# Optimization experiments

Measured on AMD Instinct MI355X. Metric: run time of the kernel, lower is better.

## Reference

```python
import jax, jax.numpy as jnp
import numpy as np


def setup_inputs() -> dict:
    key = jax.random.key(0)
    k1, k2, k3, k4, k5, k6 = jax.random.split(key, 6)
    B, V = 128, 128000
    logits = jax.random.normal(k1, (B, V), dtype=jnp.float32) * 2.0
    # keep temperatures away from 0 to avoid overflow in logits/temp
    temperatures = 0.7 + 0.6 * jax.random.uniform(k2, (B,), dtype=jnp.float32)
    top_ks = jax.random.randint(k3, (B,), 1, 1024, dtype=jnp.int32)
    top_ps = 0.7 + 0.29 * jax.random.uniform(k4, (B,), dtype=jnp.float32)
    min_ps = 0.02 * jax.random.uniform(k5, (B,), dtype=jnp.float32)
    # uniform variate for inverse-CDF multinomial sampling (one sample per row)
    u = jax.random.uniform(k6, (B, 1), dtype=jnp.float32)
    return {
        "logits": logits,
        "temperatures": temperatures,
        "top_ks": top_ks,
        "top_ps": top_ps,
        "min_ps": min_ps,
        "u": u,
    }


def reference(logits, temperatures, top_ks, top_ps, min_ps, u):
    """Faithful jax version of Sampler's torch-native sampling path:
    softmax(logits/T) -> descending sort -> top-k mask -> top-p mask
    (cumsum computed pre-mask, exactly as torch code) -> min-p mask ->
    multinomial sample (inverse CDF with provided uniform u) ->
    gather original token index. Also returns the renormalized filtered
    probs scattered back to vocab order (top_p_normalize_probs-style)."""
    B, V = logits.shape
    probs = jax.nn.softmax(logits / temperatures[:, None], axis=-1)  # [B, V]

    order = jnp.argsort(-probs, axis=-1)                     # descending indices
    probs_sort = jnp.take_along_axis(probs, order, axis=-1)  # [B, V] sorted desc
    probs_sum = jnp.cumsum(probs_sort, axis=-1)              # cumsum BEFORE masking

    pos = jnp.arange(V, dtype=jnp.int32)[None, :]
    # top-k: zero everything at rank >= top_k
    probs_sort = jnp.where(pos >= top_ks[:, None], 0.0, probs_sort)
    # top-p: zero where cumulative mass strictly before this token exceeds top_p
    probs_sort = jnp.where(probs_sum - probs_sort > top_ps[:, None], 0.0, probs_sort)
    # min-p: threshold relative to the max prob (rank-0 entry survives both masks)
    min_p_thr = probs_sort[:, :1] * min_ps[:, None]
    probs_sort = jnp.where(probs_sort < min_p_thr, 0.0, probs_sort)

    total = jnp.sum(probs_sort, axis=-1, keepdims=True)      # [B, 1]
    cdf = jnp.cumsum(probs_sort, axis=-1) / total            # normalized CDF
    # inverse-CDF sampling == torch.multinomial(probs_sort, 1)
    sampled_rank = jnp.clip(jnp.sum(cdf < u, axis=-1, keepdims=True), 0, V - 1)
    token_ids = jnp.take_along_axis(order, sampled_rank, axis=-1)[:, 0].astype(jnp.int32)

    # scatter renormalized filtered probs back to original vocab positions
    inv_order = jnp.argsort(order, axis=-1)
    norm_probs = jnp.take_along_axis(probs_sort / total, inv_order, axis=-1)
    return token_ids, norm_probs
```

## Files before the change

### kernel.cpp

```cpp
#include <hip/hip_runtime.h>
#include <stdint.h>
#include <math.h>

#define T0 256
#define T1 512
#define TPB 1024
#define NB 2048
#define SPLIT 8
#define NW 8
#define LW 256
#define NSEG (SPLIT*NW)
#define CAND2 2048
#define PS0 2048
#define L2E 1.44269504088896f

typedef float vfloat4 __attribute__((ext_vector_type(4)));
typedef unsigned long long ull;

__device__ __forceinline__ unsigned fkey(float f) {
    unsigned u = __float_as_uint(f);
    return (u & 0x80000000u) ? ~u : (u | 0x80000000u);
}
__device__ __forceinline__ float funkey(unsigned k) {
    unsigned u = (k & 0x80000000u) ? (k ^ 0x80000000u) : ~k;
    return __uint_as_float(u);
}
__device__ __forceinline__ ull packkv(unsigned k, unsigned idx) {
    return ((ull)k << 32) | (ull)(~idx);
}

__device__ __forceinline__ void suffix_scan_2048(unsigned* h, unsigned* wscr, int tid)
{
    const int lane = tid & 63, w = tid >> 6;
    const int i0 = 2047 - 2 * tid;
    const int i1 = 2046 - 2 * tid;
    unsigned a = h[i0], b = h[i1];
    unsigned s = a + b;
    unsigned inc = s;
    #pragma unroll
    for (int d = 1; d < 64; d <<= 1) { unsigned o = __shfl_up(inc, d); if (lane >= d) inc += o; }
    if (lane == 63) wscr[w] = inc;
    __syncthreads();
    if (w == 0) {
        unsigned v = (lane < 16) ? wscr[lane] : 0u;
        unsigned vi = v;
        #pragma unroll
        for (int d = 1; d < 16; d <<= 1) { unsigned o = __shfl_up(vi, d); if (lane >= d) vi += o; }
        if (lane < 16) wscr[16 + lane] = vi - v;
    }
    __syncthreads();
    unsigned off = wscr[16 + w] + (inc - s);
    h[i0] = off + a;
    h[i1] = off + a + b;
    __syncthreads();
}

__global__ __launch_bounds__(T0)
void k0_cut(const float* __restrict__ logits,
            const float* __restrict__ temps,
            const int* __restrict__ top_ks,
            float* __restrict__ ws_cy,
            unsigned* __restrict__ ws_cut,
            int V, int Vq)
{
    const int slot = blockIdx.x;
    const int b = slot / SPLIT, s = slot % SPLIT;
    const int tid = threadIdx.x, lane = tid & 63, w = tid >> 6;
    const int start = s * Vq;
    const int len = min(Vq, V - start);

    __shared__ unsigned hist[NB];
    __shared__ unsigned uscr[16];
    __shared__ float fred[8];
    __shared__ int bstar;

    if (len <= 0) {
        if (tid == 0) { ws_cut[slot] = 0xFFFFFFFFu; ws_cy[slot] = -1e30f; }
        return;
    }
    for (int i = tid; i < NB; i += T0) hist[i] = 0;
    if (tid == 0) bstar = 0;
    __syncthreads();

    const float* __restrict__ row = logits + (size_t)b * V + start;
    const vfloat4* __restrict__ row4 = (const vfloat4*)row;
    const int nps = min(len, PS0);
    const int np4 = nps >> 2;

    float m0 = -1e30f;
    for (int i = tid; i < np4; i += T0) {
        vfloat4 v = row4[i];
        #pragma unroll
        for (int j = 0; j < 4; ++j) {
            float lv = v[j];
            m0 = fmaxf(m0, lv);
            atomicAdd(&hist[fkey(lv) >> 21], 1u);
        }
    }
    for (int i = (np4 << 2) + tid; i < nps; i += T0) {
        float lv = row[i];
        m0 = fmaxf(m0, lv);
        atomicAdd(&hist[fkey(lv) >> 21], 1u);
    }
    #pragma unroll
    for (int d = 32; d > 0; d >>= 1) m0 = fmaxf(m0, __shfl_down(m0, d));
    if (lane == 0) fred[w] = m0;
    __syncthreads();
    if (tid == 0) {
        float mm = fred[0];
        for (int j = 1; j < T0 / 64; ++j) mm = fmaxf(mm, fred[j]);
        fred[4] = mm;
    }
    __syncthreads();
    const float m0max = fred[4];

    unsigned sloc[8];
    unsigned acc = 0;
    #pragma unroll
    for (int j = 0; j < 8; ++j) { acc += hist[2047 - (8 * tid + j)]; sloc[j] = acc; }
    __syncthreads();
    unsigned inc = acc;
    #pragma unroll
    for (int d = 1; d < 64; d <<= 1) { unsigned o = __shfl_up(inc, d); if (lane >= d) inc += o; }
    if (lane == 63) uscr[w] = inc;
    __syncthreads();
    if (tid == 0) {
        unsigned o = 0;
        for (int j = 0; j < T0 / 64; ++j) { unsigned t = uscr[j]; uscr[8 + j] = o; o += t; }
    }
    __syncthreads();
    unsigned off = uscr[8 + w] + (inc - acc);
    #pragma unroll
    for (int j = 0; j < 8; ++j) hist[2047 - (8 * tid + j)] = off + sloc[j];
    __syncthreads();

    int K = top_ks[b]; K = max(K, 1); K = min(K, 1024);
    float sexp = (float)K * (float)nps / (float)V;
    unsigned TGT = (unsigned)(sexp + 6.0f * sqrtf(sexp) + 16.5f);
    if (TGT > (unsigned)nps) TGT = (unsigned)nps;
    for (int e = tid; e < NB; e += T0) {
        unsigned Se = hist[e];
        unsigned Sn = (e < NB - 1) ? hist[e + 1] : 0u;
        if (Se >= TGT && Sn < TGT) bstar = e;
    }
    __syncthreads();
    if (tid == 0) {
        ws_cut[slot] = (unsigned)bstar << 21;
        ws_cy[slot]  = m0max / temps[b];
    }
}

__global__ __launch_bounds__(T1)
void k1_scan(const float* __restrict__ logits,
             const float* __restrict__ temps,
             float* __restrict__ out_probs,
             const float* __restrict__ ws_cy,
             const unsigned* __restrict__ ws_cut,
             float* __restrict__ ws_z,
             unsigned* __restrict__ ws_wcnt,
             unsigned* __restrict__ ws_maxk,
             ull* __restrict__ ws_cand,
             int V, int Vq)
{
    const int slot = blockIdx.x;
    const int b = slot / SPLIT, s = slot % SPLIT;
    const int tid = threadIdx.x, lane = tid & 63, wv = tid >> 6;
    const int start = s * Vq;
    const int len = min(Vq, V - start);

    __shared__ float fred[2 * NW];
    __shared__ unsigned ucnt[NW];

    if (len <= 0) {
        if (lane == 0) ws_wcnt[slot * NW + wv] = 0u;
        if (tid == 0) { ws_z[slot] = 0.0f; ws_maxk[slot] = 0u; }
        return;
    }

    const float invT = 1.0f / temps[b];
    const float Cy = ws_cy[slot];
    const float cutval = funkey(ws_cut[slot]);

    const float* __restrict__ row = logits + (size_t)b * V + start;
    const vfloat4* __restrict__ row4 = (const vfloat4*)row;
    const int L4 = len >> 2;

    {
        float* __restrict__ orow = out_probs + (size_t)b * V + start;
        vfloat4* __restrict__ orow4 = (vfloat4*)orow;
        const vfloat4 z4 = (vfloat4)0.0f;
        for (int i = tid; i < L4; i += T1) orow4[i] = z4;
        for (int i = (L4 << 2) + tid; i < len; i += T1) orow[i] = 0.0f;
    }

    const float ca = invT * L2E;
    const float cb = -Cy * L2E;
    ull* gw = ws_cand + ((size_t)slot * NW + wv) * LW;
    const ull lmask = (1ull << lane) - 1ull;

    unsigned wcnt = 0;
    float z0 = 0.0f, z1 = 0.0f, z2 = 0.0f, z3 = 0.0f, mb = -1e30f;

    #define E4(v) (exp2f(fmaf((v)[0], ca, cb)) + exp2f(fmaf((v)[1], ca, cb)) \
                 + exp2f(fmaf((v)[2], ca, cb)) + exp2f(fmaf((v)[3], ca, cb)))
    #define GE1(x, gi) do {                                                 \
        bool p = (x) >= cutval;                                             \
        ull bm = __ballot(p);                                               \
        if (bm) {                                                           \
            mb = fmaxf(mb, p ? (x) : -1e30f);                               \
            unsigned pos = wcnt + (unsigned)__popcll(bm & lmask);           \
            if (p && pos < LW) gw[pos] = packkv(fkey(x), (unsigned)(gi));   \
            wcnt += (unsigned)__popcll(bm);                                 \
        }                                                                   \
    } while (0)
    #define GE4(v, ii) do {                                                 \
        unsigned gbase = (unsigned)(start + ((ii) << 2));                   \
        GE1((v)[0], gbase + 0); GE1((v)[1], gbase + 1);                     \
        GE1((v)[2], gbase + 2); GE1((v)[3], gbase + 3);                     \
    } while (0)

    int k = 0;
    for (; (k + 4) * T1 <= L4; k += 4) {
        int i0 = k * T1 + tid;
        vfloat4 va = row4[i0];
        vfloat4 vb = row4[i0 + T1];
        vfloat4 vc = row4[i0 + 2 * T1];
        vfloat4 vd = row4[i0 + 3 * T1];
        z0 += E4(va); z1 += E4(vb); z2 += E4(vc); z3 += E4(vd);
        GE4(va, i0); GE4(vb, i0 + T1); GE4(vc, i0 + 2 * T1); GE4(vd, i0 + 3 * T1);
    }
    for (; k * T1 + (wv << 6) < L4; ++k) {
        int idx = k * T1 + tid;
        vfloat4 v = (idx < L4) ? row4[idx] : (vfloat4)(-1e30f);
        z0 += E4(v);
        GE4(v, idx);
    }
    for (int j = (L4 << 2) + tid; j < len; j += T1) {
        float lv = row[j];
        z0 += exp2f(fmaf(lv, ca, cb));
        GE1(lv, start + j);
    }
    #undef E4
    #undef GE1
    #undef GE4

    float z = (z0 + z1) + (z2 + z3);
    #pragma unroll
    for (int d = 32; d > 0; d >>= 1) {
        z += __shfl_down(z, d);
        mb = fmaxf(mb, __shfl_down(mb, d));
    }
    if (lane == 0) {
        fred[wv] = z; fred[NW + wv] = mb; ucnt[wv] = wcnt;
        ws_wcnt[slot * NW + wv] = wcnt;
    }
    __syncthreads();
    if (tid == 0) {
        float zz = 0.0f, mm = -1e30f; unsigned tot = 0;
        for (int j = 0; j < NW; ++j) { zz += fred[j]; mm = fmaxf(mm, fred[NW + j]); tot += ucnt[j]; }
        ws_z[slot] = zz;
        ws_maxk[slot] = tot ? fkey(mm) : 0u;
    }
}

__global__ __launch_bounds__(TPB)
void k2_sample(const float* __restrict__ logits,
               const float* __restrict__ temps,
               const int* __restrict__ top_ks,
               const float* __restrict__ top_ps,
               const float* __restrict__ min_ps,
               const float* __restrict__ uvec,
               const float* __restrict__ ws_cy,
               const float* __restrict__ ws_z,
               const unsigned* __restrict__ ws_cut,
               const unsigned* __restrict__ ws_wcnt,
               const unsigned* __restrict__ ws_maxk,
               const ull* __restrict__ ws_cand,
               float* __restrict__ out_tok,
               float* __restrict__ out_probs,
               int V)
{
    const int b = blockIdx.x;
    const int tid = threadIdx.x, lane = tid & 63, w = tid >> 6;
    const float invT = 1.0f / temps[b];
    int Korig = top_ks[b]; Korig = max(Korig, 1); Korig = min(Korig, 1024);
    const unsigned Ku = (unsigned)Korig;
    const float top_p = top_ps[b], min_p = min_ps[b], uval = uvec[b];

    __shared__ __align__(16) char smem[53760];
    ull*            cand  = (ull*)(smem);
    ull*            cand2 = (ull*)(smem + 16384);
    unsigned*       hist  = (unsigned*)(smem + 32768);
    unsigned short* cnts  = (unsigned short*)(smem + 41216);
    float*          sh_p  = (float*)(smem + 45312);
    float*          sh_c  = (float*)(smem + 49408);
    unsigned short* segc  = (unsigned short*)(smem + 53504);
    __shared__ unsigned uscr[32];
    __shared__ float fws[32];
    __shared__ unsigned scnt;
    __shared__ int sh_i1, sh_i2;
    __shared__ unsigned sh_u1;

    bool myfb = false;
    for (int i = tid; i < NSEG; i += TPB) {
        unsigned c = ws_wcnt[b * NSEG + i];
        if (c > (unsigned)LW) myfb = true;
        segc[i] = (unsigned short)min(c, (unsigned)LW);
    }
    float Cy[SPLIT], zq[SPLIT];
    unsigned cutq[SPLIT], mkq[SPLIT];
    #pragma unroll
    for (int q = 0; q < SPLIT; ++q) {
        int sl = b * SPLIT + q;
        Cy[q] = ws_cy[sl]; zq[q] = ws_z[sl];
        cutq[q] = ws_cut[sl]; mkq[q] = ws_maxk[sl];
    }
    __syncthreads();
    unsigned cntq[SPLIT];
    #pragma unroll
    for (int q = 0; q < SPLIT; ++q) {
        unsigned t = 0;
        #pragma unroll
        for (int v = 0; v < NW; ++v) t += segc[q * NW + v];
        cntq[q] = t;
    }
    float Y = -1e30f;
    #pragma unroll
    for (int q = 0; q < SPLIT; ++q) if (zq[q] > 0.0f) Y = fmaxf(Y, Cy[q]);
    float Z = 0.0f;
    #pragma unroll
    for (int q = 0; q < SPLIT; ++q)
        if (zq[q] > 0.0f) Z += zq[q] * exp2f((Cy[q] - Y) * L2E);

    unsigned cutmax = 0, mincut = 0xFFFFFFFFu, maxkey = 0;
    #pragma unroll
    for (int q = 0; q < SPLIT; ++q) {
        if (cntq[q] > 0u) {
            if (!isfinite(zq[q])) myfb = true;
            cutmax = max(cutmax, cutq[q]);
            mincut = min(mincut, cutq[q]);
            maxkey = max(maxkey, mkq[q]);
        }
    }
    if (mincut == 0xFFFFFFFFu || !isfinite(Z) || Z <= 0.0f) myfb = true;
    bool fb = __syncthreads_or((int)myfb) != 0;

    unsigned Tkeyb = 0;
    int count = 0, bstar = 0, shift = 0;
    const unsigned base = mincut;
    const ull* cbase = ws_cand + (size_t)b * NSEG * LW;

    if (!fb) {
        const unsigned range = maxkey - base;
        while ((range >> shift) > (unsigned)(NB - 1)) shift++;
        for (int i = tid; i <= NB; i += TPB) hist[i] = 0;
        if (tid == 0) { sh_i1 = -1; scnt = 0; }
        __syncthreads();
        for (int v = tid; v < NSEG * LW; v += TPB) {
            int off = v & (LW - 1);
            int seg = v >> 8;
            if (off < (int)segc[seg]) {
                ull e = cbase[v];
                atomicAdd(&hist[((unsigned)(e >> 32) - base) >> shift], 1u);
            }
        }
        __syncthreads();
        unsigned fat = 0;
        for (int i = tid; i < NB; i += TPB) {
            unsigned h = hist[i];
            cnts[i] = (unsigned short)h;
            fat = max(fat, h);
        }
        #pragma unroll
        for (int d = 32; d > 0; d >>= 1) fat = max(fat, __shfl_down(fat, d));
        if (lane == 0) uscr[w] = fat;
        __syncthreads();
        if (tid == 0) {
            unsigned m2 = 0;
            for (int j = 0; j < 16; ++j) m2 = max(m2, uscr[j]);
            uscr[16] = m2;
        }
        __syncthreads();
        if (uscr[16] > 64u) fb = true;
    }
    if (!fb) {
        suffix_scan_2048(hist, uscr, tid);
        for (int e = tid; e < NB; e += TPB) {
            unsigned Se = hist[e], Sn = (e < NB - 1) ? hist[e + 1] : 0u;
            if (Se >= Ku && Sn < Ku) { sh_i1 = e; sh_u1 = Se; }
        }
        __syncthreads();
        if (sh_i1 < 0) fb = true;
        else {
            bstar = sh_i1;
            count = (int)sh_u1;
            Tkeyb = base + ((unsigned)bstar << shift);
            if (Tkeyb < cutmax || count > CAND2) fb = true;
        }
    }
    if (!fb) {
        for (int v = tid; v < NSEG * LW; v += TPB) {
            int off = v & (LW - 1);
            int seg = v >> 8;
            if (off < (int)segc[seg]) {
                ull e = cbase[v];
                unsigned k = (unsigned)(e >> 32);
                if (k >= Tkeyb) {
                    unsigned bin = (k - base) >> shift;
                    unsigned pos = atomicAdd(&hist[bin + 1], 1u);
                    cand2[pos] = e;
                }
            }
        }
        __syncthreads();
        for (int e = bstar + tid; e < NB; e += TPB) {
            int c = (int)cnts[e];
            if (c >= 2) {
                int st = (int)hist[e + 1] - c;
                for (int x = 1; x < c; ++x) {
                    ull key = cand2[st + x];
                    int y = x - 1;
                    while (y >= 0 && cand2[st + y] < key) { cand2[st + y + 1] = cand2[st + y]; --y; }
                    cand2[st + y + 1] = key;
                }
            }
        }
        __syncthreads();
    }

    if (fb) {
        const float* __restrict__ row = logits + (size_t)b * V;
        float m = -1e30f, z = 0.0f;
        for (int i = tid; i < V; i += TPB) {
            float y = row[i] * invT;
            float nm = fmaxf(m, y);
            z = z * exp2f((m - nm) * L2E) + exp2f((y - nm) * L2E);
            m = nm;
        }
        sh_p[tid] = m; sh_c[tid] = z;
        __syncthreads();
        for (int d = TPB >> 1; d > 0; d >>= 1) {
            if (tid < d) {
                float m1 = sh_p[tid], z1 = sh_c[tid];
                float m2 = sh_p[tid + d], z2 = sh_c[tid + d];
                float mm = fmaxf(m1, m2);
                sh_c[tid] = z1 * exp2f((m1 - mm) * L2E) + z2 * exp2f((m2 - mm) * L2E);
                sh_p[tid] = mm;
            }
            __syncthreads();
        }
        Y = sh_p[0]; Z = sh_c[0];
        __syncthreads();
        for (int i = tid; i < NB; i += TPB) hist[i] = 0;
        if (tid == 0) { sh_i1 = 0; sh_i2 = 0; sh_u1 = 0; }
        __syncthreads();
        for (int i = tid; i < V; i += TPB) atomicAdd(&hist[fkey(row[i]) >> 21], 1u);
        __syncthreads();
        suffix_scan_2048(hist, uscr, tid);
        for (int e = tid; e < NB; e += TPB) {
            unsigned Se = hist[e], Sn = (e < NB-1) ? hist[e+1] : 0u;
            if (Se >= Ku && Sn < Ku) { sh_i1 = e; sh_u1 = Sn; }
        }
        __syncthreads();
        int b1 = sh_i1;
        unsigned cab = sh_u1;
        for (int i = tid; i < NB; i += TPB) hist[i] = 0;
        __syncthreads();
        for (int i = tid; i < V; i += TPB) {
            unsigned k = fkey(row[i]);
            if ((int)(k >> 21) == b1) atomicAdd(&hist[(k >> 10) & (NB - 1)], 1u);
        }
        __syncthreads();
        suffix_scan_2048(hist, uscr, tid);
        for (int e = tid; e < NB; e += TPB) {
            unsigned Se = cab + hist[e];
            unsigned Sn = cab + ((e < NB-1) ? hist[e+1] : 0u);
            if (Se >= Ku && Sn < Ku) sh_i2 = e;
        }
        __syncthreads();
        unsigned Tkey = ((unsigned)b1 << 21) | ((unsigned)sh_i2 << 10);
        if (tid == 0) scnt = 0;
        __syncthreads();
        for (int i = tid; i < V; i += TPB) {
            unsigned k = fkey(row[i]);
            if (k >= Tkey) {
                unsigned pos = atomicAdd(&scnt, 1u);
                if (pos < CAND2) cand[pos] = packkv(k, (unsigned)i);
            }
        }
        __syncthreads();
        count = (scnt < (unsigned)CAND2) ? (int)scnt : CAND2;

        int n_sort = 1;
        while (n_sort < count) n_sort <<= 1;
        for (int i = tid; i < n_sort; i += TPB)
            if (i >= count) cand[i] = 0ull;
        __syncthreads();
        for (int kk = 2; kk <= n_sort; kk <<= 1) {
            for (int j = kk >> 1; j > 0; j >>= 1) {
                for (int i = tid; i < n_sort; i += TPB) {
                    int ixj = i ^ j;
                    if (ixj > i) {
                        ull a = cand[i], c = cand[ixj];
                        bool up = (i & kk) == 0;
                        if (up ? (a < c) : (a > c)) { cand[i] = c; cand[ixj] = a; }
                    }
                }
                __syncthreads();
            }
        }
    }

    ull* srt = fb ? cand : cand2;
    int K = min(Korig, count);

    float pv = 0.0f;
    if (tid < K) {
        unsigned k = (unsigned)(srt[tid] >> 32);
        pv = exp2f((funkey(k) * invT - Y) * L2E) / Z;
    }
    float inc = pv;
    #pragma unroll
    for (int d = 1; d < 64; d <<= 1) { float o = __shfl_up(inc, d); if (lane >= d) inc += o; }
    if (lane == 63) fws[w] = inc;
    __syncthreads();
    if (w == 0) {
        float v = (lane < 16) ? fws[lane] : 0.0f;
        float vi = v;
        #pragma unroll
        for (int d = 1; d < 16; d <<= 1) { float o = __shfl_up(vi, d); if (lane >= d) vi += o; }
        if (lane < 16) fws[16 + lane] = vi - v;
    }
    __syncthreads();
    float cum = inc + fws[16 + w];
    sh_p[tid] = pv;
    sh_c[tid] = cum;
    if (tid == 0) sh_i1 = K;
    __syncthreads();

    if (tid < K) {
        float excl = cum - pv;
        if (excl > top_p) atomicMin(&sh_i1, tid);
    }
    __syncthreads();
    int n1 = sh_i1;
    float thr = sh_p[0] * min_p;
    if (tid == 0) sh_i2 = n1;
    __syncthreads();
    if (tid < n1 && sh_p[tid] < thr) atomicMin(&sh_i2, tid);
    __syncthreads();
    int nf = sh_i2;
    float total = sh_c[nf - 1];

    int pred = (tid < nf) && ((sh_c[tid] / total) < uval);
    int rank = __syncthreads_count(pred);
    if (rank > nf - 1) rank = nf - 1;
    if (rank < 0) rank = 0;
    if (tid == 0)
        out_tok[b] = (float)(~(unsigned)(srt[rank] & 0xFFFFFFFFull));

    if (tid < nf) {
        unsigned idx = ~(unsigned)(srt[tid] & 0xFFFFFFFFull);
        out_probs[(size_t)b * V + idx] = sh_p[tid] / total;
    }
}

extern "C" void kernel_launch(void* const* d_in, const int* in_sizes, int n_in,
                              void* d_out, int out_size, void* d_ws, size_t ws_size,
                              hipStream_t stream) {
    const float* logits = (const float*)d_in[0];
    const float* temps  = (const float*)d_in[1];
    const int*   top_ks = (const int*)d_in[2];
    const float* top_ps = (const float*)d_in[3];
    const float* min_ps = (const float*)d_in[4];
    const float* u      = (const float*)d_in[5];
    const int B = in_sizes[1];
    const int V = in_sizes[0] / B;
    float* out_tok   = (float*)d_out;
    float* out_probs = out_tok + B;

    int Vq = (((V + SPLIT - 1) / SPLIT) + 3) & ~3;

    char* ws = (char*)d_ws;
    size_t off = 0;
    auto take = [&](size_t bytes) { char* p = ws + off; off = (off + bytes + 255) & ~(size_t)255; return p; };
    float*    ws_cy   = (float*)take((size_t)B * SPLIT * sizeof(float));
    float*    ws_z    = (float*)take((size_t)B * SPLIT * sizeof(float));
    unsigned* ws_cut  = (unsigned*)take((size_t)B * SPLIT * sizeof(unsigned));
    unsigned* ws_wcnt = (unsigned*)take((size_t)B * NSEG * sizeof(unsigned));
    unsigned* ws_maxk = (unsigned*)take((size_t)B * SPLIT * sizeof(unsigned));
    ull*      ws_cand = (ull*)take((size_t)B * NSEG * LW * sizeof(ull));
    (void)ws_size;

    k0_cut<<<dim3(SPLIT * B), dim3(T0), 0, stream>>>(
        logits, temps, top_ks, ws_cy, ws_cut, V, Vq);
    k1_scan<<<dim3(SPLIT * B), dim3(T1), 0, stream>>>(
        logits, temps, out_probs, ws_cy, ws_cut, ws_z, ws_wcnt, ws_maxk, ws_cand, V, Vq);
    k2_sample<<<dim3(B), dim3(TPB), 0, stream>>>(
        logits, temps, top_ks, top_ps, min_ps, u, ws_cy, ws_z, ws_cut, ws_wcnt,
        ws_maxk, ws_cand, out_tok, out_probs, V);
}
```

Baseline: 158.3 us.

## Fuse three sampling kernels into one with last-block-arrives finalization

Merges the cut-histogram, scan and per-row sampling kernels into a single kernel. Each row is now split across 4 blocks of 1024 threads instead of 8, and the last block to arrive on a per-row atomic counter performs the top-k/top-p/min-p sampling. The pre-pass histogram uses a larger prefix and the zero-fill of output probs uses nontemporal stores. This removes two kernel launches and the inter-kernel gaps, at the cost of a memset launch, per-block threadfences, and the sample stage running on only one block per row.

```diff
diff --git a/kernel.cpp b/kernel.cpp
--- a/kernel.cpp
+++ b/kernel.cpp
@@ -2,16 +2,14 @@
 #include <stdint.h>
 #include <math.h>
 
-#define T0 256
-#define T1 512
-#define TPB 1024
+#define T 1024
 #define NB 2048
-#define SPLIT 8
-#define NW 8
+#define SPLIT 4
+#define NW 16
 #define LW 256
 #define NSEG (SPLIT*NW)
 #define CAND2 2048
-#define PS0 2048
+#define PS 4096
 #define L2E 1.44269504088896f
 
 typedef float vfloat4 __attribute__((ext_vector_type(4)));
@@ -55,254 +53,200 @@
     __syncthreads();
 }
 
-__global__ __launch_bounds__(T0)
-void k0_cut(const float* __restrict__ logits,
-            const float* __restrict__ temps,
-            const int* __restrict__ top_ks,
-            float* __restrict__ ws_cy,
-            unsigned* __restrict__ ws_cut,
-            int V, int Vq)
-{
-    const int slot = blockIdx.x;
-    const int b = slot / SPLIT, s = slot % SPLIT;
-    const int tid = threadIdx.x, lane = tid & 63, w = tid >> 6;
-    const int start = s * Vq;
-    const int len = min(Vq, V - start);
-
-    __shared__ unsigned hist[NB];
-    __shared__ unsigned uscr[16];
-    __shared__ float fred[8];
-    __shared__ int bstar;
-
-    if (len <= 0) {
-        if (tid == 0) { ws_cut[slot] = 0xFFFFFFFFu; ws_cy[slot] = -1e30f; }
-        return;
-    }
-    for (int i = tid; i < NB; i += T0) hist[i] = 0;
-    if (tid == 0) bstar = 0;
-    __syncthreads();
-
-    const float* __restrict__ row = logits + (size_t)b * V + start;
-    const vfloat4* __restrict__ row4 = (const vfloat4*)row;
-    const int nps = min(len, PS0);
-    const int np4 = nps >> 2;
-
-    float m0 = -1e30f;
-    for (int i = tid; i < np4; i += T0) {
-        vfloat4 v = row4[i];
-        #pragma unroll
-        for (int j = 0; j < 4; ++j) {
-            float lv = v[j];
-            m0 = fmaxf(m0, lv);
-            atomicAdd(&hist[fkey(lv) >> 21], 1u);
-        }
-    }
-    for (int i = (np4 << 2) + tid; i < nps; i += T0) {
-        float lv = row[i];
-        m0 = fmaxf(m0, lv);
-        atomicAdd(&hist[fkey(lv) >> 21], 1u);
-    }
-    #pragma unroll
-    for (int d = 32; d > 0; d >>= 1) m0 = fmaxf(m0, __shfl_down(m0, d));
-    if (lane == 0) fred[w] = m0;
-    __syncthreads();
-    if (tid == 0) {
-        float mm = fred[0];
-        for (int j = 1; j < T0 / 64; ++j) mm = fmaxf(mm, fred[j]);
-        fred[4] = mm;
-    }
-    __syncthreads();
-    const float m0max = fred[4];
-
-    unsigned sloc[8];
-    unsigned acc = 0;
-    #pragma unroll
-    for (int j = 0; j < 8; ++j) { acc += hist[2047 - (8 * tid + j)]; sloc[j] = acc; }
-    __syncthreads();
-    unsigned inc = acc;
-    #pragma unroll
-    for (int d = 1; d < 64; d <<= 1) { unsigned o = __shfl_up(inc, d); if (lane >= d) inc += o; }
-    if (lane == 63) uscr[w] = inc;
-    __syncthreads();
-    if (tid == 0) {
-        unsigned o = 0;
-        for (int j = 0; j < T0 / 64; ++j) { unsigned t = uscr[j]; uscr[8 + j] = o; o += t; }
-    }
-    __syncthreads();
-    unsigned off = uscr[8 + w] + (inc - acc);
-    #pragma unroll
-    for (int j = 0; j < 8; ++j) hist[2047 - (8 * tid + j)] = off + sloc[j];
-    __syncthreads();
-
-    int K = top_ks[b]; K = max(K, 1); K = min(K, 1024);
-    float sexp = (float)K * (float)nps / (float)V;
-    unsigned TGT = (unsigned)(sexp + 6.0f * sqrtf(sexp) + 16.5f);
-    if (TGT > (unsigned)nps) TGT = (unsigned)nps;
-    for (int e = tid; e < NB; e += T0) {
-        unsigned Se = hist[e];
-        unsigned Sn = (e < NB - 1) ? hist[e + 1] : 0u;
-        if (Se >= TGT && Sn < TGT) bstar = e;
-    }
-    __syncthreads();
-    if (tid == 0) {
-        ws_cut[slot] = (unsigned)bstar << 21;
-        ws_cy[slot]  = m0max / temps[b];
-    }
-}
-
-__global__ __launch_bounds__(T1)
-void k1_scan(const float* __restrict__ logits,
-             const float* __restrict__ temps,
-             float* __restrict__ out_probs,
-             const float* __restrict__ ws_cy,
-             const unsigned* __restrict__ ws_cut,
-             float* __restrict__ ws_z,
-             unsigned* __restrict__ ws_wcnt,
-             unsigned* __restrict__ ws_maxk,
-             ull* __restrict__ ws_cand,
-             int V, int Vq)
+__global__ __launch_bounds__(T, 8)
+void fused(const float* __restrict__ logits,
+           const float* __restrict__ temps,
+           const int* __restrict__ top_ks,
+           const float* __restrict__ top_ps,
+           const float* __restrict__ min_ps,
+           const float* __restrict__ uvec,
+           unsigned* __restrict__ ws_arrive,
+           float* __restrict__ ws_cy,
+           float* __restrict__ ws_z,
+           unsigned* __restrict__ ws_cut,
+           unsigned* __restrict__ ws_wcnt,
+           unsigned* __restrict__ ws_maxk,
+           ull* __restrict__ ws_cand,
+           float* __restrict__ out_tok,
+           float* __restrict__ out_probs,
+           int V, int Vq, int B)
 {
     const int slot = blockIdx.x;
     const int b = slot / SPLIT, s = slot % SPLIT;
     const int tid = threadIdx.x, lane = tid & 63, wv = tid >> 6;
     const int start = s * Vq;
     const int len = min(Vq, V - start);
-
+    const float invT = 1.0f / temps[b];
+
+    __shared__ __align__(16) char smem[37120];
+    ull*            cand2 = (ull*)smem;
+    unsigned*       hist  = (unsigned*)(smem + 16384);
+    unsigned short* cnts  = (unsigned short*)(smem + 24584);
+    float*          sh_p  = (float*)(smem + 28680);
+    float*          sh_c  = (float*)(smem + 32776);
+    unsigned short* segc  = (unsigned short*)(smem + 36872);
+    __shared__ unsigned uscr[32];
+    __shared__ float fws[32];
     __shared__ float fred[2 * NW];
     __shared__ unsigned ucnt[NW];
-
-    if (len <= 0) {
+    __shared__ unsigned scnt;
+    __shared__ int sh_i1, sh_i2, sh_win;
+    __shared__ unsigned sh_u1;
+
+    float cutval = 1e30f; float Cy_loc = -1e30f; unsigned cutkey = 0xFFFFFFFFu;
+    if (len > 0) {
+        for (int i = tid; i < NB; i += T) hist[i] = 0;
+        if (tid == 0) sh_i1 = 0;
+        __syncthreads();
+        const float* __restrict__ row = logits + (size_t)b * V + start;
+        const vfloat4* __restrict__ row4 = (const vfloat4*)row;
+        const int nps = min(len, PS);
+        const int np4 = nps >> 2;
+        float m0 = -1e30f;
+        for (int i = tid; i < np4; i += T) {
+            vfloat4 v = row4[i];
+            #pragma unroll
+            for (int j = 0; j < 4; ++j) {
+                float lv = v[j];
+                m0 = fmaxf(m0, lv);
+                atomicAdd(&hist[fkey(lv) >> 21], 1u);
+            }
+        }
+        for (int i = (np4 << 2) + tid; i < nps; i += T) {
+            float lv = row[i];
+            m0 = fmaxf(m0, lv);
+            atomicAdd(&hist[fkey(lv) >> 21], 1u);
+        }
+        #pragma unroll
+        for (int d = 32; d > 0; d >>= 1) m0 = fmaxf(m0, __shfl_down(m0, d));
+        if (lane == 0) fred[wv] = m0;
+        __syncthreads();
+        if (tid == 0) {
+            float mm = fred[0];
+            for (int j = 1; j < NW; ++j) mm = fmaxf(mm, fred[j]);
+            fws[0] = mm;
+        }
+        __syncthreads();
+        const float m0max = fws[0];
+        suffix_scan_2048(hist, uscr, tid);
+        int K = top_ks[b]; K = max(K, 1); K = min(K, 1024);
+        float sexp = (float)K * (float)nps / (float)V;
+        unsigned TGT = (unsigned)(sexp + 6.0f * sqrtf(sexp) + 16.5f);
+        if (TGT > (unsigned)nps) TGT = (unsigned)nps;
+        for (int e = tid; e < NB; e += T) {
+            unsigned Se = hist[e];
+            unsigned Sn = (e < NB - 1) ? hist[e + 1] : 0u;
+            if (Se >= TGT && Sn < TGT) sh_i1 = e;
+        }
+        __syncthreads();
+        cutkey = (unsigned)sh_i1 << 21;
+        cutval = funkey(cutkey);
+        Cy_loc = m0max * invT;
+        if (tid == 0) { ws_cut[slot] = cutkey; ws_cy[slot] = Cy_loc; }
+    } else {
+        if (tid == 0) { ws_cut[slot] = 0xFFFFFFFFu; ws_cy[slot] = -1e30f; }
+    }
+
+    if (len > 0) {
+        const float* __restrict__ row = logits + (size_t)b * V + start;
+        const vfloat4* __restrict__ row4 = (const vfloat4*)row;
+        const int L4 = len >> 2;
+        {
+            float* __restrict__ orow = out_probs + (size_t)b * V + start;
+            vfloat4* __restrict__ orow4 = (vfloat4*)orow;
+            const vfloat4 z4 = (vfloat4)0.0f;
+            for (int i = tid; i < L4; i += T) __builtin_nontemporal_store(z4, &orow4[i]);
+            for (int i = (L4 << 2) + tid; i < len; i += T) __builtin_nontemporal_store(0.0f, &orow[i]);
+        }
+        const float ca = invT * L2E;
+        const float cb = -Cy_loc * L2E;
+        ull* gw = ws_cand + ((size_t)slot * NW + wv) * LW;
+        const ull lmask = (1ull << lane) - 1ull;
+        unsigned wcnt = 0;
+        float z0 = 0.0f, z1 = 0.0f, z2 = 0.0f, z3 = 0.0f, mb = -1e30f;
+
+        #define E4(v) (exp2f(fmaf((v)[0], ca, cb)) + exp2f(fmaf((v)[1], ca, cb)) \
+                     + exp2f(fmaf((v)[2], ca, cb)) + exp2f(fmaf((v)[3], ca, cb)))
+        #define GE1(x, gi) do {                                                 \
+            bool p = (x) >= cutval;                                             \
+            ull bm = __ballot(p);                                               \
+            if (bm) {                                                           \
+                mb = fmaxf(mb, p ? (x) : -1e30f);                               \
+                unsigned pos = wcnt + (unsigned)__popcll(bm & lmask);           \
+                if (p && pos < LW) gw[pos] = packkv(fkey(x), (unsigned)(gi));   \
+                wcnt += (unsigned)__popcll(bm);                                 \
+            }                                                                   \
+        } while (0)
+        #define GE4(v, ii) do {                                                 \
+            unsigned gbase = (unsigned)(start + ((ii) << 2));                   \
+            GE1((v)[0], gbase + 0); GE1((v)[1], gbase + 1);                     \
+            GE1((v)[2], gbase + 2); GE1((v)[3], gbase + 3);                     \
+        } while (0)
+
+        int k = 0;
+        for (; (k + 4) * T <= L4; k += 4) {
+            int i0 = k * T + tid;
+            vfloat4 va = row4[i0];
+            vfloat4 vb = row4[i0 + T];
+            vfloat4 vc = row4[i0 + 2 * T];
+            vfloat4 vd = row4[i0 + 3 * T];
+            z0 += E4(va); z1 += E4(vb); z2 += E4(vc); z3 += E4(vd);
+            GE4(va, i0); GE4(vb, i0 + T); GE4(vc, i0 + 2 * T); GE4(vd, i0 + 3 * T);
+        }
+        for (; k * T + (wv << 6) < L4; ++k) {
+            int idx = k * T + tid;
+            vfloat4 v = (idx < L4) ? row4[idx] : (vfloat4)(-1e30f);
+            z0 += E4(v);
+            GE4(v, idx);
+        }
+        for (int j = (L4 << 2) + tid; j < len; j += T) {
+            float lv = row[j];
+            z0 += exp2f(fmaf(lv, ca, cb));
+            GE1(lv, start + j);
+        }
+        #undef E4
+        #undef GE1
+        #undef GE4
+
+        float z = (z0 + z1) + (z2 + z3);
+        __syncthreads();
+        #pragma unroll
+        for (int d = 32; d > 0; d >>= 1) {
+            z += __shfl_down(z, d);
+            mb = fmaxf(mb, __shfl_down(mb, d));
+        }
+        if (lane == 0) {
+            fred[wv] = z; fred[NW + wv] = mb; ucnt[wv] = wcnt;
+            ws_wcnt[slot * NW + wv] = wcnt;
+        }
+        __syncthreads();
+        if (tid == 0) {
+            float zz = 0.0f, mm = -1e30f; unsigned tot = 0;
+            for (int j = 0; j < NW; ++j) { zz += fred[j]; mm = fmaxf(mm, fred[NW + j]); tot += ucnt[j]; }
+            ws_z[slot] = zz;
+            ws_maxk[slot] = tot ? fkey(mm) : 0u;
+        }
+    } else {
         if (lane == 0) ws_wcnt[slot * NW + wv] = 0u;
         if (tid == 0) { ws_z[slot] = 0.0f; ws_maxk[slot] = 0u; }
-        return;
-    }
-
-    const float invT = 1.0f / temps[b];
-    const float Cy = ws_cy[slot];
-    const float cutval = funkey(ws_cut[slot]);
-
-    const float* __restrict__ row = logits + (size_t)b * V + start;
-    const vfloat4* __restrict__ row4 = (const vfloat4*)row;
-    const int L4 = len >> 2;
-
-    {
-        float* __restrict__ orow = out_probs + (size_t)b * V + start;
-        vfloat4* __restrict__ orow4 = (vfloat4*)orow;
-        const vfloat4 z4 = (vfloat4)0.0f;
-        for (int i = tid; i < L4; i += T1) orow4[i] = z4;
-        for (int i = (L4 << 2) + tid; i < len; i += T1) orow[i] = 0.0f;
-    }
-
-    const float ca = invT * L2E;
-    const float cb = -Cy * L2E;
-    ull* gw = ws_cand + ((size_t)slot * NW + wv) * LW;
-    const ull lmask = (1ull << lane) - 1ull;
-
-    unsigned wcnt = 0;
-    float z0 = 0.0f, z1 = 0.0f, z2 = 0.0f, z3 = 0.0f, mb = -1e30f;
-
-    #define E4(v) (exp2f(fmaf((v)[0], ca, cb)) + exp2f(fmaf((v)[1], ca, cb)) \
-                 + exp2f(fmaf((v)[2], ca, cb)) + exp2f(fmaf((v)[3], ca, cb)))
-    #define GE1(x, gi) do {                                                 \
-        bool p = (x) >= cutval;                                             \
-        ull bm = __ballot(p);                                               \
-        if (bm) {                                                           \
-            mb = fmaxf(mb, p ? (x) : -1e30f);                               \
-            unsigned pos = wcnt + (unsigned)__popcll(bm & lmask);           \
-            if (p && pos < LW) gw[pos] = packkv(fkey(x), (unsigned)(gi));   \
-            wcnt += (unsigned)__popcll(bm);                                 \
-        }                                                                   \
-    } while (0)
-    #define GE4(v, ii) do {                                                 \
-        unsigned gbase = (unsigned)(start + ((ii) << 2));                   \
-        GE1((v)[0], gbase + 0); GE1((v)[1], gbase + 1);                     \
-        GE1((v)[2], gbase + 2); GE1((v)[3], gbase + 3);                     \
-    } while (0)
-
-    int k = 0;
-    for (; (k + 4) * T1 <= L4; k += 4) {
-        int i0 = k * T1 + tid;
-        vfloat4 va = row4[i0];
-        vfloat4 vb = row4[i0 + T1];
-        vfloat4 vc = row4[i0 + 2 * T1];
-        vfloat4 vd = row4[i0 + 3 * T1];
-        z0 += E4(va); z1 += E4(vb); z2 += E4(vc); z3 += E4(vd);
-        GE4(va, i0); GE4(vb, i0 + T1); GE4(vc, i0 + 2 * T1); GE4(vd, i0 + 3 * T1);
-    }
-    for (; k * T1 + (wv << 6) < L4; ++k) {
-        int idx = k * T1 + tid;
-        vfloat4 v = (idx < L4) ? row4[idx] : (vfloat4)(-1e30f);
-        z0 += E4(v);
-        GE4(v, idx);
-    }
-    for (int j = (L4 << 2) + tid; j < len; j += T1) {
-        float lv = row[j];
-        z0 += exp2f(fmaf(lv, ca, cb));
-        GE1(lv, start + j);
-    }
-    #undef E4
-    #undef GE1
-    #undef GE4
-
-    float z = (z0 + z1) + (z2 + z3);
-    #pragma unroll
-    for (int d = 32; d > 0; d >>= 1) {
-        z += __shfl_down(z, d);
-        mb = fmaxf(mb, __shfl_down(mb, d));
-    }
-    if (lane == 0) {
-        fred[wv] = z; fred[NW + wv] = mb; ucnt[wv] = wcnt;
-        ws_wcnt[slot * NW + wv] = wcnt;
-    }
-    __syncthreads();
+    }
+
+    __syncthreads();
+    __threadfence();
     if (tid == 0) {
-        float zz = 0.0f, mm = -1e30f; unsigned tot = 0;
-        for (int j = 0; j < NW; ++j) { zz += fred[j]; mm = fmaxf(mm, fred[NW + j]); tot += ucnt[j]; }
-        ws_z[slot] = zz;
-        ws_maxk[slot] = tot ? fkey(mm) : 0u;
-    }
-}
-
-__global__ __launch_bounds__(TPB)
-void k2_sample(const float* __restrict__ logits,
-               const float* __restrict__ temps,
-               const int* __restrict__ top_ks,
-               const float* __restrict__ top_ps,
-               const float* __restrict__ min_ps,
-               const float* __restrict__ uvec,
-               const float* __restrict__ ws_cy,
-               const float* __restrict__ ws_z,
-               const unsigned* __restrict__ ws_cut,
-               const unsigned* __restrict__ ws_wcnt,
-               const unsigned* __restrict__ ws_maxk,
-               const ull* __restrict__ ws_cand,
-               float* __restrict__ out_tok,
-               float* __restrict__ out_probs,
-               int V)
-{
-    const int b = blockIdx.x;
-    const int tid = threadIdx.x, lane = tid & 63, w = tid >> 6;
-    const float invT = 1.0f / temps[b];
+        unsigned old = atomicAdd(&ws_arrive[b], 1u);
+        sh_win = (old == (unsigned)(SPLIT - 1));
+    }
+    __syncthreads();
+    if (!sh_win) return;
+    __threadfence();
+
     int Korig = top_ks[b]; Korig = max(Korig, 1); Korig = min(Korig, 1024);
     const unsigned Ku = (unsigned)Korig;
     const float top_p = top_ps[b], min_p = min_ps[b], uval = uvec[b];
 
-    __shared__ __align__(16) char smem[53760];
-    ull*            cand  = (ull*)(smem);
-    ull*            cand2 = (ull*)(smem + 16384);
-    unsigned*       hist  = (unsigned*)(smem + 32768);
-    unsigned short* cnts  = (unsigned short*)(smem + 41216);
-    float*          sh_p  = (float*)(smem + 45312);
-    float*          sh_c  = (float*)(smem + 49408);
-    unsigned short* segc  = (unsigned short*)(smem + 53504);
-    __shared__ unsigned uscr[32];
-    __shared__ float fws[32];
-    __shared__ unsigned scnt;
-    __shared__ int sh_i1, sh_i2;
-    __shared__ unsigned sh_u1;
-
     bool myfb = false;
-    for (int i = tid; i < NSEG; i += TPB) {
+    for (int i = tid; i < NSEG; i += T) {
         unsigned c = ws_wcnt[b * NSEG + i];
         if (c > (unsigned)LW) myfb = true;
         segc[i] = (unsigned short)min(c, (unsigned)LW);
@@ -353,10 +297,10 @@
     if (!fb) {
         const unsigned range = maxkey - base;
         while ((range >> shift) > (unsigned)(NB - 1)) shift++;
-        for (int i = tid; i <= NB; i += TPB) hist[i] = 0;
+        for (int i = tid; i <= NB; i += T) hist[i] = 0;
         if (tid == 0) { sh_i1 = -1; scnt = 0; }
         __syncthreads();
-        for (int v = tid; v < NSEG * LW; v += TPB) {
+        for (int v = tid; v < NSEG * LW; v += T) {
             int off = v & (LW - 1);
             int seg = v >> 8;
             if (off < (int)segc[seg]) {
@@ -366,14 +310,14 @@
         }
         __syncthreads();
         unsigned fat = 0;
-        for (int i = tid; i < NB; i += TPB) {
+        for (int i = tid; i < NB; i += T) {
             unsigned h = hist[i];
             cnts[i] = (unsigned short)h;
             fat = max(fat, h);
         }
         #pragma unroll
         for (int d = 32; d > 0; d >>= 1) fat = max(fat, __shfl_down(fat, d));
-        if (lane == 0) uscr[w] = fat;
+        if (lane == 0) uscr[wv] = fat;
         __syncthreads();
         if (tid == 0) {
             unsigned m2 = 0;
@@ -385,7 +329,7 @@
     }
     if (!fb) {
         suffix_scan_2048(hist, uscr, tid);
-        for (int e = tid; e < NB; e += TPB) {
+        for (int e = tid; e < NB; e += T) {
             unsigned Se = hist[e], Sn = (e < NB - 1) ? hist[e + 1] : 0u;
             if (Se >= Ku && Sn < Ku) { sh_i1 = e; sh_u1 = Se; }
         }
@@ -399,7 +343,7 @@
         }
     }
     if (!fb) {
-        for (int v = tid; v < NSEG * LW; v += TPB) {
+        for (int v = tid; v < NSEG * LW; v += T) {
             int off = v & (LW - 1);
             int seg = v >> 8;
             if (off < (int)segc[seg]) {
@@ -413,7 +357,7 @@
             }
         }
         __syncthreads();
-        for (int e = bstar + tid; e < NB; e += TPB) {
+        for (int e = bstar + tid; e < NB; e += T) {
             int c = (int)cnts[e];
             if (c >= 2) {
                 int st = (int)hist[e + 1] - c;
@@ -431,7 +375,7 @@
     if (fb) {
         const float* __restrict__ row = logits + (size_t)b * V;
         float m = -1e30f, z = 0.0f;
-        for (int i = tid; i < V; i += TPB) {
+        for (int i = tid; i < V; i += T) {
             float y = row[i] * invT;
             float nm = fmaxf(m, y);
             z = z * exp2f((m - nm) * L2E) + exp2f((y - nm) * L2E);
@@ -439,7 +383,7 @@
         }
         sh_p[tid] = m; sh_c[tid] = z;
         __syncthreads();
-        for (int d = TPB >> 1; d > 0; d >>= 1) {
+        for (int d = T >> 1; d > 0; d >>= 1) {
             if (tid < d) {
                 float m1 = sh_p[tid], z1 = sh_c[tid];
                 float m2 = sh_p[tid + d], z2 = sh_c[tid + d];
@@ -451,41 +395,41 @@
         }
         Y = sh_p[0]; Z = sh_c[0];
         __syncthreads();
-        for (int i = tid; i < NB; i += TPB) hist[i] = 0;
+        for (int i = tid; i < NB; i += T) hist[i] = 0;
         if (tid == 0) { sh_i1 = 0; sh_i2 = 0; sh_u1 = 0; }
         __syncthreads();
-        for (int i = tid; i < V; i += TPB) atomicAdd(&hist[fkey(row[i]) >> 21], 1u);
+        for (int i = tid; i < V; i += T) atomicAdd(&hist[fkey(row[i]) >> 21], 1u);
         __syncthreads();
         suffix_scan_2048(hist, uscr, tid);
-        for (int e = tid; e < NB; e += TPB) {
-            unsigned Se = hist[e], Sn = (e < NB-1) ? hist[e+1] : 0u;
+        for (int e = tid; e < NB; e += T) {
+            unsigned Se = hist[e], Sn = (e < NB - 1) ? hist[e + 1] : 0u;
             if (Se >= Ku && Sn < Ku) { sh_i1 = e; sh_u1 = Sn; }
         }
         __syncthreads();
         int b1 = sh_i1;
         unsigned cab = sh_u1;
-        for (int i = tid; i < NB; i += TPB) hist[i] = 0;
-        __syncthreads();
-        for (int i = tid; i < V; i += TPB) {
+        for (int i = tid; i < NB; i += T) hist[i] = 0;
+        __syncthreads();
+        for (int i = tid; i < V; i += T) {
             unsigned k = fkey(row[i]);
             if ((int)(k >> 21) == b1) atomicAdd(&hist[(k >> 10) & (NB - 1)], 1u);
         }
         __syncthreads();
         suffix_scan_2048(hist, uscr, tid);
-        for (int e = tid; e < NB; e += TPB) {
+        for (int e = tid; e < NB; e += T) {
             unsigned Se = cab + hist[e];
-            unsigned Sn = cab + ((e < NB-1) ? hist[e+1] : 0u);
+            unsigned Sn = cab + ((e < NB - 1) ? hist[e + 1] : 0u);
             if (Se >= Ku && Sn < Ku) sh_i2 = e;
         }
         __syncthreads();
         unsigned Tkey = ((unsigned)b1 << 21) | ((unsigned)sh_i2 << 10);
         if (tid == 0) scnt = 0;
         __syncthreads();
-        for (int i = tid; i < V; i += TPB) {
+        for (int i = tid; i < V; i += T) {
             unsigned k = fkey(row[i]);
             if (k >= Tkey) {
                 unsigned pos = atomicAdd(&scnt, 1u);
-                if (pos < CAND2) cand[pos] = packkv(k, (unsigned)i);
+                if (pos < CAND2) cand2[pos] = packkv(k, (unsigned)i);
             }
         }
         __syncthreads();
@@ -493,17 +437,17 @@
 
         int n_sort = 1;
         while (n_sort < count) n_sort <<= 1;
-        for (int i = tid; i < n_sort; i += TPB)
-            if (i >= count) cand[i] = 0ull;
+        for (int i = tid; i < n_sort; i += T)
+            if (i >= count) cand2[i] = 0ull;
         __syncthreads();
         for (int kk = 2; kk <= n_sort; kk <<= 1) {
             for (int j = kk >> 1; j > 0; j >>= 1) {
-                for (int i = tid; i < n_sort; i += TPB) {
+                for (int i = tid; i < n_sort; i += T) {
                     int ixj = i ^ j;
                     if (ixj > i) {
-                        ull a = cand[i], c = cand[ixj];
+                        ull a = cand2[i], c = cand2[ixj];
                         bool up = (i & kk) == 0;
-                        if (up ? (a < c) : (a > c)) { cand[i] = c; cand[ixj] = a; }
+                        if (up ? (a < c) : (a > c)) { cand2[i] = c; cand2[ixj] = a; }
                     }
                 }
                 __syncthreads();
@@ -511,20 +455,19 @@
         }
     }
 
-    ull* srt = fb ? cand : cand2;
     int K = min(Korig, count);
 
     float pv = 0.0f;
     if (tid < K) {
-        unsigned k = (unsigned)(srt[tid] >> 32);
+        unsigned k = (unsigned)(cand2[tid] >> 32);
         pv = exp2f((funkey(k) * invT - Y) * L2E) / Z;
     }
     float inc = pv;
     #pragma unroll
     for (int d = 1; d < 64; d <<= 1) { float o = __shfl_up(inc, d); if (lane >= d) inc += o; }
-    if (lane == 63) fws[w] = inc;
-    __syncthreads();
-    if (w == 0) {
+    if (lane == 63) fws[wv] = inc;
+    __syncthreads();
+    if (wv == 0) {
         float v = (lane < 16) ? fws[lane] : 0.0f;
         float vi = v;
         #pragma unroll
@@ -532,7 +475,7 @@
         if (lane < 16) fws[16 + lane] = vi - v;
     }
     __syncthreads();
-    float cum = inc + fws[16 + w];
+    float cum = inc + fws[16 + wv];
     sh_p[tid] = pv;
     sh_c[tid] = cum;
     if (tid == 0) sh_i1 = K;
@@ -557,10 +500,10 @@
     if (rank > nf - 1) rank = nf - 1;
     if (rank < 0) rank = 0;
     if (tid == 0)
-        out_tok[b] = (float)(~(unsigned)(srt[rank] & 0xFFFFFFFFull));
+        out_tok[b] = (float)(~(unsigned)(cand2[rank] & 0xFFFFFFFFull));
 
     if (tid < nf) {
-        unsigned idx = ~(unsigned)(srt[tid] & 0xFFFFFFFFull);
+        unsigned idx = ~(unsigned)(cand2[tid] & 0xFFFFFFFFull);
         out_probs[(size_t)b * V + idx] = sh_p[tid] / total;
     }
 }
@@ -574,8 +517,8 @@
     const float* top_ps = (const float*)d_in[3];
     const float* min_ps = (const float*)d_in[4];
     const float* u      = (const float*)d_in[5];
-    const int B = in_sizes[1];
-    const int V = in_sizes[0] / B;
+    int B = in_sizes[1];
+    int V = in_sizes[0] / B;
     float* out_tok   = (float*)d_out;
     float* out_probs = out_tok + B;
 
@@ -584,6 +527,7 @@
     char* ws = (char*)d_ws;
     size_t off = 0;
     auto take = [&](size_t bytes) { char* p = ws + off; off = (off + bytes + 255) & ~(size_t)255; return p; };
+    unsigned* ws_arrive = (unsigned*)take((size_t)B * sizeof(unsigned));
     float*    ws_cy   = (float*)take((size_t)B * SPLIT * sizeof(float));
     float*    ws_z    = (float*)take((size_t)B * SPLIT * sizeof(float));
     unsigned* ws_cut  = (unsigned*)take((size_t)B * SPLIT * sizeof(unsigned));
@@ -592,11 +536,10 @@
     ull*      ws_cand = (ull*)take((size_t)B * NSEG * LW * sizeof(ull));
     (void)ws_size;
 
-    k0_cut<<<dim3(SPLIT * B), dim3(T0), 0, stream>>>(
-        logits, temps, top_ks, ws_cy, ws_cut, V, Vq);
-    k1_scan<<<dim3(SPLIT * B), dim3(T1), 0, stream>>>(
-        logits, temps, out_probs, ws_cy, ws_cut, ws_z, ws_wcnt, ws_maxk, ws_cand, V, Vq);
-    k2_sample<<<dim3(B), dim3(TPB), 0, stream>>>(
-        logits, temps, top_ks, top_ps, min_ps, u, ws_cy, ws_z, ws_cut, ws_wcnt,
-        ws_maxk, ws_cand, out_tok, out_probs, V);
+    hipMemsetAsync(ws_arrive, 0, (size_t)B * sizeof(unsigned), stream);
+
+    fused<<<dim3(SPLIT * B), dim3(T), 0, stream>>>(
+        logits, temps, top_ks, top_ps, min_ps, u,
+        ws_arrive, ws_cy, ws_z, ws_cut, ws_wcnt, ws_maxk, ws_cand,
+        out_tok, out_probs, V, Vq, B);
 }
```

After: 442.4 us. 2.79x slower.
